# Optimization experiments

Hardware: AMD Instinct MI355X
Metric: run time of the kernel (lower is better)

Reference implementation:

```python
import jax, jax.numpy as jnp
import numpy as np

P = 16  # patch size

def _conv1x1(w, b, h):
    # w: [O, C], h: [B, C, H, W]
    return jnp.einsum('oc,bcij->boij', w, h) + b[None, :, None, None]

def _forward(x, pe_w, pe_b, mix1_w, mix1_b, mix2_w, mix2_b, qc_w, qc_b,
             codebook, dpre1_w, dpre1_b, dpre2_w, dpre2_b, up_w, up_b):
    B, Cin, H, W = x.shape
    Hp, Wp = H // P, W // P
    # --- encoder: non-overlapping patchify conv (kernel=stride=P) ---
    xp = x.reshape(B, Cin, Hp, P, Wp, P)
    h = jnp.einsum('bcipjq,ocpq->boij', xp, pe_w) + pe_b[None, :, None, None]
    h = jax.nn.relu(h)
    h = jax.nn.relu(_conv1x1(mix1_w, mix1_b, h))
    h = _conv1x1(mix2_w, mix2_b, h)
    # quantize_conv_b
    e = _conv1x1(qc_w, qc_b, h)                      # [B, D, Hp, Wp]
    D = e.shape[1]
    z = e.transpose(0, 2, 3, 1).reshape(B, Hp * Wp, D)   # [B, N, D]
    # --- vector quantization: euclidean argmin over codebook ---
    # dist[b,n,k] = |z|^2 - 2 z.c_k + |c_k|^2
    dist = ((z * z).sum(-1, keepdims=True)
            - 2.0 * jnp.einsum('bnd,kd->bnk', z, codebook)
            + (codebook * codebook).sum(-1))
    idx = jnp.argmin(dist, axis=-1)                  # [B, N] int
    q = codebook[idx]                                # [B, N, D]
    # commitment loss (quantize detached, as in VectorQuantize)
    diff = jnp.mean(jnp.square(jax.lax.stop_gradient(q) - z))
    # straight-through estimator
    q = z + jax.lax.stop_gradient(q - z)
    quant = q.reshape(B, Hp, Wp, D).transpose(0, 3, 1, 2)  # [B, D, Hp, Wp]
    # --- decoder ---
    h = jax.nn.relu(_conv1x1(dpre1_w, dpre1_b, quant))
    h = jax.nn.relu(_conv1x1(dpre2_w, dpre2_b, h))
    # unpatchify: ConvTranspose2d kernel=stride=P, torch weight [C, out, P, P]
    Cout = up_w.shape[1]
    dec = jnp.einsum('bcij,copq->boipjq', h, up_w).reshape(B, Cout, Hp * P, Wp * P)
    dec = dec + up_b[None, :, None, None]
    return dec, diff[None], idx

def setup_inputs() -> dict:
    key = jax.random.key(0)
    ks = jax.random.split(key, 16)
    B, Cin, H, W = 32, 3, 256, 256
    C, D, K = 256, 512, 8192
    s = 0.02
    f32 = jnp.float32
    return {
        'x':       jax.random.normal(ks[0], (B, Cin, H, W), f32),
        'pe_w':    jax.random.normal(ks[1], (C, Cin, P, P), f32) * s,
        'pe_b':    jnp.zeros((C,), f32),
        'mix1_w':  jax.random.normal(ks[2], (C, C), f32) * s,
        'mix1_b':  jnp.zeros((C,), f32),
        'mix2_w':  jax.random.normal(ks[3], (C, C), f32) * s,
        'mix2_b':  jnp.zeros((C,), f32),
        'qc_w':    jax.random.normal(ks[4], (D, C), f32) * s,
        'qc_b':    jnp.zeros((D,), f32),
        'codebook': jax.random.normal(ks[5], (K, D), f32),
        'dpre1_w': jax.random.normal(ks[6], (C, D), f32) * s,
        'dpre1_b': jnp.zeros((C,), f32),
        'dpre2_w': jax.random.normal(ks[7], (C, C), f32) * s,
        'dpre2_b': jnp.zeros((C,), f32),
        'up_w':    jax.random.normal(ks[8], (C, Cin, P, P), f32) * s,
        'up_b':    jnp.zeros((Cin,), f32),
    }

def reference(x, pe_w, pe_b, mix1_w, mix1_b, mix2_w, mix2_b, qc_w, qc_b,
              codebook, dpre1_w, dpre1_b, dpre2_w, dpre2_b, up_w, up_b):
    return _forward(x, pe_w, pe_b, mix1_w, mix1_b, mix2_w, mix2_b, qc_w, qc_b,
                    codebook, dpre1_w, dpre1_b, dpre2_w, dpre2_b, up_w, up_b)
```

## Files before the change

kernel.cpp:

```cpp
#include <hip/hip_runtime.h>
#include <hip/hip_bf16.h>
#include <float.h>


#define TOK   8192
#define CBK   8192
#define CBD   512

typedef short  short8v __attribute__((ext_vector_type(8)));
typedef float  f32x4   __attribute__((ext_vector_type(4)));

__device__ __forceinline__ unsigned short f2bf(float x) {
    union { __hip_bfloat16 b; unsigned short u; } c;
    c.b = __float2bfloat16(x);
    return c.u;
}
__device__ __forceinline__ float bf2f(unsigned short h) {
    return __uint_as_float((unsigned)h << 16);
}

template<int NPASS, int AMODE, int STMODE, bool RELU>
__global__ __launch_bounds__(256)
void gemm_mfma(const float* __restrict__ A, const float* __restrict__ Bw,
               const float* __restrict__ bias, float* __restrict__ C,
               const float* __restrict__ rowidx, int M, int N, int K)
{
    __shared__ __align__(16) unsigned short Az[2][128 * 64];
    __shared__ __align__(16) unsigned short Bc[2][64 * 64];

    const int tid = threadIdx.x, lane = tid & 63, wid = tid >> 6;
    const int wr = wid >> 1, wc = wid & 1;
    const int m0 = blockIdx.x * 128, n0 = blockIdx.y * 64;
    const int l15 = lane & 15, l4 = lane >> 4;

    size_t abase[4];
    #pragma unroll
    for (int it = 0; it < 4; ++it) {
        const int m = m0 + it * 32 + (tid >> 3);
        if constexpr (AMODE == 1) {
            const int b = m >> 8, i = (m >> 4) & 15, j = m & 15;
            abase[it] = (size_t)b * 196608 + i * 4096 + j * 16;
        } else if constexpr (AMODE == 2) {
            abase[it] = (size_t)((int)rowidx[m]) * K;
        } else {
            abase[it] = (size_t)m * K;
        }
    }

    f32x4 acc[4][2];
    #pragma unroll
    for (int mi = 0; mi < 4; ++mi)
        #pragma unroll
        for (int nj = 0; nj < 2; ++nj)
            acc[mi][nj] = (f32x4){0.f, 0.f, 0.f, 0.f};

    for (int k0 = 0; k0 < K; k0 += 64) {
        __syncthreads();
        #pragma unroll
        for (int it = 0; it < 4; ++it) {
            const int ci = it * 256 + tid;
            const int r = ci >> 3, cb8 = ci & 7;
            const int kk = k0 + cb8 * 8;
            const float* src;
            if constexpr (AMODE == 1) {
                const int c = kk >> 8, p = (kk >> 4) & 15, q = kk & 15;
                src = A + abase[it] + (size_t)c * 65536 + p * 256 + q;
            } else {
                src = A + abase[it] + kk;
            }
            const float4 f0 = *(const float4*)src;
            const float4 f1 = *(const float4*)(src + 4);
            const float fs[8] = {f0.x, f0.y, f0.z, f0.w, f1.x, f1.y, f1.z, f1.w};
            union { unsigned short u[8]; short8v v; } H, L;
            #pragma unroll
            for (int j = 0; j < 8; ++j) {
                const unsigned short h = f2bf(fs[j]);
                H.u[j] = h;
                L.u[j] = f2bf(fs[j] - bf2f(h));
            }
            const int off = r * 64 + ((cb8 ^ (r & 7)) << 3);
            *(short8v*)(&Az[0][off]) = H.v;
            *(short8v*)(&Az[1][off]) = L.v;
        }
        #pragma unroll
        for (int it = 0; it < 2; ++it) {
            const int ci = it * 256 + tid;
            const int r = ci >> 3, cb8 = ci & 7;
            const float* src = Bw + (size_t)(n0 + r) * K + k0 + cb8 * 8;
            const float4 f0 = *(const float4*)src;
            const float4 f1 = *(const float4*)(src + 4);
            const float fs[8] = {f0.x, f0.y, f0.z, f0.w, f1.x, f1.y, f1.z, f1.w};
            union { unsigned short u[8]; short8v v; } H, L;
            #pragma unroll
            for (int j = 0; j < 8; ++j) {
                const unsigned short h = f2bf(fs[j]);
                H.u[j] = h;
                L.u[j] = f2bf(fs[j] - bf2f(h));
            }
            const int off = r * 64 + ((cb8 ^ (r & 7)) << 3);
            *(short8v*)(&Bc[0][off]) = H.v;
            *(short8v*)(&Bc[1][off]) = L.v;
        }
        __syncthreads();

        #pragma unroll
        for (int ks = 0; ks < 2; ++ks) {
            short8v aFh[4], aFl[4];
            #pragma unroll
            for (int mi = 0; mi < 4; ++mi) {
                const int r = wr * 64 + mi * 16 + l15;
                const int off = r * 64 + (((ks * 4 + l4) ^ (r & 7)) << 3);
                aFh[mi] = *(const short8v*)(&Az[0][off]);
                aFl[mi] = *(const short8v*)(&Az[1][off]);
            }
            #pragma unroll
            for (int nj = 0; nj < 2; ++nj) {
                const int rn = wc * 32 + nj * 16 + l15;
                const int off = rn * 64 + (((ks * 4 + l4) ^ (rn & 7)) << 3);
                const short8v bh = *(const short8v*)(&Bc[0][off]);
                const short8v bl = *(const short8v*)(&Bc[1][off]);
                #pragma unroll
                for (int mi = 0; mi < 4; ++mi) {
                    acc[mi][nj] = __builtin_amdgcn_mfma_f32_16x16x32_bf16(aFh[mi], bh, acc[mi][nj], 0, 0, 0);
                    acc[mi][nj] = __builtin_amdgcn_mfma_f32_16x16x32_bf16(aFh[mi], bl, acc[mi][nj], 0, 0, 0);
                    acc[mi][nj] = __builtin_amdgcn_mfma_f32_16x16x32_bf16(aFl[mi], bh, acc[mi][nj], 0, 0, 0);
                    if constexpr (NPASS == 4)
                        acc[mi][nj] = __builtin_amdgcn_mfma_f32_16x16x32_bf16(aFl[mi], bl, acc[mi][nj], 0, 0, 0);
                }
            }
        }
    }

    #pragma unroll
    for (int nj = 0; nj < 2; ++nj) {
        const int n = n0 + wc * 32 + nj * 16 + l15;
        const float bv = (STMODE == 0) ? bias[n] : bias[n >> 8];
        #pragma unroll
        for (int mi = 0; mi < 4; ++mi) {
            #pragma unroll
            for (int i = 0; i < 4; ++i) {
                const int m = m0 + wr * 64 + mi * 16 + l4 * 4 + i;
                float v = acc[mi][nj][i] + bv;
                if constexpr (RELU) v = fmaxf(v, 0.f);
                if constexpr (STMODE == 0) {
                    C[(size_t)m * N + n] = v;
                } else {
                    const int o = n >> 8, p = (n >> 4) & 15, q = n & 15;
                    const int b = m >> 8, ii = (m >> 4) & 15, jj = m & 15;
                    C[((size_t)(b * 3 + o) * 256 + ii * 16 + p) * 256 + jj * 16 + q] = v;
                }
            }
        }
    }
}

__global__ __launch_bounds__(256)
void cb_norm(const float* __restrict__ cb, float* __restrict__ cnorm)
{
    const int row  = blockIdx.x * 4 + (threadIdx.x >> 6);
    const int lane = threadIdx.x & 63;
    const float4* p = (const float4*)(cb + (size_t)row * CBD + lane * 8);
    const float4 a = p[0], b = p[1];
    double s = (double)a.x*a.x + (double)a.y*a.y + (double)a.z*a.z + (double)a.w*a.w
             + (double)b.x*b.x + (double)b.y*b.y + (double)b.z*b.z + (double)b.w*b.w;
    #pragma unroll
    for (int off = 32; off >= 1; off >>= 1) s += __shfl_down(s, off);
    if (lane == 0) cnorm[row] = (float)s;
}

__global__ __launch_bounds__(256)
void split_bf16_h(const float* __restrict__ src, unsigned short* __restrict__ hi)
{
    const size_t i8 = (size_t)blockIdx.x * 256 + threadIdx.x;
    const float4 a = *(const float4*)(src + i8 * 8);
    const float4 b = *(const float4*)(src + i8 * 8 + 4);
    const float xs[8] = {a.x, a.y, a.z, a.w, b.x, b.y, b.z, b.w};
    union { unsigned short u[8]; short8v v; } H;
    #pragma unroll
    for (int j = 0; j < 8; ++j) H.u[j] = f2bf(xs[j]);
    *(short8v*)(hi + i8 * 8) = H.v;
}

#define NSY 8
#define CPB (CBK / NSY)
#define NCAND 32

__global__ __launch_bounds__(256)
void vq_mfma1(const unsigned short* __restrict__ zh, const unsigned short* __restrict__ cbh,
              const float* __restrict__ cnorm, int* __restrict__ cand)
{
    __shared__ __align__(16) unsigned short Az[128 * 64];
    __shared__ __align__(16) unsigned short Bc[128 * 64];

    const int tid = threadIdx.x, lane = tid & 63, wid = tid >> 6;
    const int wr = wid >> 1, wc = wid & 1;
    const int m0 = blockIdx.x * 128;
    const int l15 = lane & 15, l4 = lane >> 4;

    float r1[16], r2[16];
    int   i1[16], i2[16];
    #pragma unroll
    for (int r = 0; r < 16; ++r) { r1[r] = FLT_MAX; r2[r] = FLT_MAX; i1[r] = 0; i2[r] = 0; }

    for (int chk = 0; chk < CPB / 128; ++chk) {
        const int c0 = blockIdx.y * CPB + chk * 128;

        f32x4 acc[4][4];
        #pragma unroll
        for (int mi = 0; mi < 4; ++mi)
            #pragma unroll
            for (int nj = 0; nj < 4; ++nj)
                acc[mi][nj] = (f32x4){0.f, 0.f, 0.f, 0.f};

        for (int k0 = 0; k0 < CBD; k0 += 64) {
            __syncthreads();
            #pragma unroll
            for (int it = 0; it < 4; ++it) {
                const int ci = it * 256 + tid;
                const int r = ci >> 3, cb8 = ci & 7;
                const int off = r * 64 + ((cb8 ^ (r & 7)) << 3);
                *(short8v*)(&Az[off]) =
                    *(const short8v*)(zh + (size_t)(m0 + r) * CBD + k0 + cb8 * 8);
                *(short8v*)(&Bc[off]) =
                    *(const short8v*)(cbh + (size_t)(c0 + r) * CBD + k0 + cb8 * 8);
            }
            __syncthreads();

            #pragma unroll
            for (int ks = 0; ks < 2; ++ks) {
                short8v aF[4];
                #pragma unroll
                for (int mi = 0; mi < 4; ++mi) {
                    const int r = wr * 64 + mi * 16 + l15;
                    aF[mi] = *(const short8v*)(&Az[r * 64 + (((ks * 4 + l4) ^ (r & 7)) << 3)]);
                }
                #pragma unroll
                for (int nj = 0; nj < 4; ++nj) {
                    const int rn = wc * 64 + nj * 16 + l15;
                    const short8v bF = *(const short8v*)(&Bc[rn * 64 + (((ks * 4 + l4) ^ (rn & 7)) << 3)]);
                    #pragma unroll
                    for (int mi = 0; mi < 4; ++mi)
                        acc[mi][nj] = __builtin_amdgcn_mfma_f32_16x16x32_bf16(aF[mi], bF, acc[mi][nj], 0, 0, 0);
                }
            }
        }

        #pragma unroll
        for (int nj = 0; nj < 4; ++nj) {
            const int code = c0 + wc * 64 + nj * 16 + l15;
            const float cn = cnorm[code];
            #pragma unroll
            for (int mi = 0; mi < 4; ++mi) {
                #pragma unroll
                for (int i = 0; i < 4; ++i) {
                    const float d = cn - 2.0f * acc[mi][nj][i];
                    const int rr = mi * 4 + i;
                    if (d < r1[rr]) { r2[rr] = r1[rr]; i2[rr] = i1[rr]; r1[rr] = d; i1[rr] = code; }
                    else if (d < r2[rr]) { r2[rr] = d; i2[rr] = code; }
                }
            }
        }
    }

    #pragma unroll
    for (int r = 0; r < 16; ++r) {
        float a1 = r1[r], a2 = r2[r];
        int   x1 = i1[r], x2 = i2[r];
        #pragma unroll
        for (int off = 1; off < 16; off <<= 1) {
            const float b1 = __shfl_xor(a1, off), b2 = __shfl_xor(a2, off);
            const int   y1 = __shfl_xor(x1, off), y2 = __shfl_xor(x2, off);
            if (b1 < a1) {
                const float n2 = (a1 < b2) ? a1 : b2;
                const int   m2 = (a1 < b2) ? x1 : y2;
                a2 = n2; x2 = m2; a1 = b1; x1 = y1;
            } else {
                if (b1 < a2) { a2 = b1; x2 = y1; }
            }
        }
        r1[r] = a1; i1[r] = x1; r2[r] = a2; i2[r] = x2;
    }
    if (l15 == 0) {
        const int slot = blockIdx.y * 2 + wc;
        #pragma unroll
        for (int mi = 0; mi < 4; ++mi)
            #pragma unroll
            for (int i = 0; i < 4; ++i) {
                const int tok = m0 + wr * 64 + mi * 16 + l4 * 4 + i;
                cand[(slot * 2 + 0) * TOK + tok] = i1[mi * 4 + i];
                cand[(slot * 2 + 1) * TOK + tok] = i2[mi * 4 + i];
            }
    }
}

__global__ __launch_bounds__(256)
void exact_select(const float* __restrict__ z, const float* __restrict__ cb,
                  const int* __restrict__ cand, int ncand,
                  float* __restrict__ idx_out, float* __restrict__ diffp)
{
    const int t    = blockIdx.x * 4 + (threadIdx.x >> 6);
    const int lane = threadIdx.x & 63;

    const float4 za = *(const float4*)(z + (size_t)t * CBD + lane * 8);
    const float4 zb = *(const float4*)(z + (size_t)t * CBD + lane * 8 + 4);
    const double zd[8] = {za.x, za.y, za.z, za.w, zb.x, zb.y, zb.z, zb.w};

    double bestd = DBL_MAX;
    int    besti = 0x7fffffff;
    for (int c = 0; c < ncand; ++c) {
        const int code = cand[c * TOK + t];
        const float4 ca  = *(const float4*)(cb + (size_t)code * CBD + lane * 8);
        const float4 cbv = *(const float4*)(cb + (size_t)code * CBD + lane * 8 + 4);
        const double cd[8] = {ca.x, ca.y, ca.z, ca.w, cbv.x, cbv.y, cbv.z, cbv.w};
        double s = 0.0;
        #pragma unroll
        for (int j = 0; j < 8; ++j) { const double d = cd[j] - zd[j]; s = fma(d, d, s); }
        #pragma unroll
        for (int off = 32; off >= 1; off >>= 1) s += __shfl_down(s, off);
        s = __shfl(s, 0);
        if (s < bestd || (s == bestd && code < besti)) { bestd = s; besti = code; }
    }
    if (lane == 0) {
        idx_out[t] = (float)besti;
        atomicAdd(diffp, (float)(bestd * (1.0 / ((double)TOK * CBD))));
    }
}

__global__ __launch_bounds__(256)
void transpose_upw(const float* __restrict__ up_w, float* __restrict__ upT)
{
    const int id = blockIdx.x * 256 + threadIdx.x;
    const int n = id >> 8, c = id & 255;
    upT[id] = up_w[c * 768 + n];
}

extern "C" void kernel_launch(void* const* d_in, const int* in_sizes, int n_in,
                              void* d_out, int out_size, void* d_ws, size_t ws_size,
                              hipStream_t stream)
{
    const float* x        = (const float*)d_in[0];
    const float* pe_w     = (const float*)d_in[1];
    const float* pe_b     = (const float*)d_in[2];
    const float* mix1_w   = (const float*)d_in[3];
    const float* mix1_b   = (const float*)d_in[4];
    const float* mix2_w   = (const float*)d_in[5];
    const float* mix2_b   = (const float*)d_in[6];
    const float* qc_w     = (const float*)d_in[7];
    const float* qc_b     = (const float*)d_in[8];
    const float* codebook = (const float*)d_in[9];
    const float* dpre1_w  = (const float*)d_in[10];
    const float* dpre1_b  = (const float*)d_in[11];
    const float* dpre2_w  = (const float*)d_in[12];
    const float* dpre2_b  = (const float*)d_in[13];
    const float* up_w     = (const float*)d_in[14];
    const float* up_b     = (const float*)d_in[15];

    float* ws = (float*)d_ws;
    float* h1    = ws;
    float* h2    = ws + 2097152;
    float* z     = ws + 4194304;
    float* upT   = ws + 8388608;
    float* cnorm = ws + 8585216;
    int*   cand  = (int*)(ws + 8593408);
    unsigned short* zh  = (unsigned short*)(ws + 8855552);
    unsigned short* cbh = (unsigned short*)(ws + 10952704);

    float* dec     = (float*)d_out;
    float* diffp   = dec + 6291456;
    float* idx_out = (float*)d_out + 6291457;

    transpose_upw<<<768, 256, 0, stream>>>(up_w, upT);
    cb_norm<<<CBK / 4, 256, 0, stream>>>(codebook, cnorm);
    split_bf16_h<<<2048, 256, 0, stream>>>(codebook, cbh);

    gemm_mfma<4, 1, 0, true ><<<dim3(64, 4),  256, 0, stream>>>(x,  pe_w,   pe_b,   h1, nullptr, TOK, 256, 768);
    gemm_mfma<4, 0, 0, true ><<<dim3(64, 4),  256, 0, stream>>>(h1, mix1_w, mix1_b, h2, nullptr, TOK, 256, 256);
    gemm_mfma<4, 0, 0, false><<<dim3(64, 4),  256, 0, stream>>>(h2, mix2_w, mix2_b, h1, nullptr, TOK, 256, 256);
    gemm_mfma<4, 0, 0, false><<<dim3(64, 8),  256, 0, stream>>>(h1, qc_w,   qc_b,   z,  nullptr, TOK, 512, 256);

    split_bf16_h<<<2048, 256, 0, stream>>>(z, zh);
    vq_mfma1<<<dim3(TOK / 128, NSY), 256, 0, stream>>>(zh, cbh, cnorm, cand);
    hipMemsetAsync(diffp, 0, sizeof(float), stream);
    exact_select<<<TOK / 4, 256, 0, stream>>>(z, codebook, cand, NCAND, idx_out, diffp);

    gemm_mfma<3, 2, 0, true ><<<dim3(64, 4),  256, 0, stream>>>(codebook, dpre1_w, dpre1_b, h1, idx_out, TOK, 256, 512);
    gemm_mfma<3, 0, 0, true ><<<dim3(64, 4),  256, 0, stream>>>(h1, dpre2_w, dpre2_b, h2, nullptr, TOK, 256, 256);
    gemm_mfma<3, 0, 1, false><<<dim3(64, 12), 256, 0, stream>>>(h2, upT, up_b, dec, nullptr, TOK, 768, 256);
}
```

Measured before the change: 720.7 us.

## Pre-split operands to bf16 hi/lo and double-buffer GEMMs with direct global-to-LDS loads

```diff
diff --git a/kernel.cpp b/kernel.cpp
--- a/kernel.cpp
+++ b/kernel.cpp
@@ -9,6 +9,7 @@
 
 typedef short  short8v __attribute__((ext_vector_type(8)));
 typedef float  f32x4   __attribute__((ext_vector_type(4)));
+typedef unsigned short ush;
 
 __device__ __forceinline__ unsigned short f2bf(float x) {
     union { __hip_bfloat16 b; unsigned short u; } c;
@@ -19,33 +20,65 @@
     return __uint_as_float((unsigned)h << 16);
 }
 
+__device__ __forceinline__ void gload16(const void* g, void* l) {
+    __builtin_amdgcn_global_load_lds(
+        (const __attribute__((address_space(1))) unsigned int*)g,
+        (__attribute__((address_space(3))) unsigned int*)l, 16, 0, 0);
+}
+
 template<int NPASS, int AMODE, int STMODE, bool RELU>
 __global__ __launch_bounds__(256)
-void gemm_mfma(const float* __restrict__ A, const float* __restrict__ Bw,
-               const float* __restrict__ bias, float* __restrict__ C,
-               const float* __restrict__ rowidx, int M, int N, int K)
-{
-    __shared__ __align__(16) unsigned short Az[2][128 * 64];
-    __shared__ __align__(16) unsigned short Bc[2][64 * 64];
+void gemm_bf2(const ush* __restrict__ Ah, const ush* __restrict__ Al,
+              const ush* __restrict__ Bh, const ush* __restrict__ Bl,
+              const float* __restrict__ bias,
+              float* __restrict__ Cf, ush* __restrict__ Ch, ush* __restrict__ Cl,
+              const float* __restrict__ rowidx, int N, int K, int NT)
+{
+    __shared__ __align__(16) ush AzH[2][128 * 64];
+    __shared__ __align__(16) ush AzL[2][128 * 64];
+    __shared__ __align__(16) ush BcH[2][64 * 64];
+    __shared__ __align__(16) ush BcL[2][64 * 64];
 
     const int tid = threadIdx.x, lane = tid & 63, wid = tid >> 6;
     const int wr = wid >> 1, wc = wid & 1;
     const int m0 = blockIdx.x * 128, n0 = blockIdx.y * 64;
     const int l15 = lane & 15, l4 = lane >> 4;
 
-    size_t abase[4];
-    #pragma unroll
-    for (int it = 0; it < 4; ++it) {
-        const int m = m0 + it * 32 + (tid >> 3);
-        if constexpr (AMODE == 1) {
-            const int b = m >> 8, i = (m >> 4) & 15, j = m & 15;
-            abase[it] = (size_t)b * 196608 + i * 4096 + j * 16;
-        } else if constexpr (AMODE == 2) {
-            abase[it] = (size_t)((int)rowidx[m]) * K;
-        } else {
-            abase[it] = (size_t)m * K;
-        }
-    }
+    size_t aoff[4];
+    int    aldst[4];
+    #pragma unroll
+    for (int i = 0; i < 4; ++i) {
+        const int ci = (wid * 4 + i) * 64 + lane;
+        const int r = ci >> 3, p = ci & 7;
+        size_t rowbase;
+        if constexpr (AMODE == 2) rowbase = (size_t)((int)rowidx[m0 + r]) * K;
+        else                      rowbase = (size_t)(m0 + r) * K;
+        aoff[i]  = rowbase + ((p ^ (r & 7)) << 3);
+        aldst[i] = (wid * 4 + i) * 512;
+    }
+    size_t boff[2];
+    int    bldst[2];
+    #pragma unroll
+    for (int i = 0; i < 2; ++i) {
+        const int ci = (wid * 2 + i) * 64 + lane;
+        const int r = ci >> 3, p = ci & 7;
+        boff[i]  = (size_t)(n0 + r) * K + ((p ^ (r & 7)) << 3);
+        bldst[i] = (wid * 2 + i) * 512;
+    }
+
+    auto STAGE = [&](int t, int b) {
+        const int k0 = t << 6;
+        #pragma unroll
+        for (int i = 0; i < 4; ++i) {
+            gload16(Ah + aoff[i] + k0, &AzH[b][aldst[i]]);
+            gload16(Al + aoff[i] + k0, &AzL[b][aldst[i]]);
+        }
+        #pragma unroll
+        for (int i = 0; i < 2; ++i) {
+            gload16(Bh + boff[i] + k0, &BcH[b][bldst[i]]);
+            gload16(Bl + boff[i] + k0, &BcL[b][bldst[i]]);
+        }
+    };
 
     f32x4 acc[4][2];
     #pragma unroll
@@ -54,55 +87,11 @@
         for (int nj = 0; nj < 2; ++nj)
             acc[mi][nj] = (f32x4){0.f, 0.f, 0.f, 0.f};
 
-    for (int k0 = 0; k0 < K; k0 += 64) {
-        __syncthreads();
-        #pragma unroll
-        for (int it = 0; it < 4; ++it) {
-            const int ci = it * 256 + tid;
-            const int r = ci >> 3, cb8 = ci & 7;
-            const int kk = k0 + cb8 * 8;
-            const float* src;
-            if constexpr (AMODE == 1) {
-                const int c = kk >> 8, p = (kk >> 4) & 15, q = kk & 15;
-                src = A + abase[it] + (size_t)c * 65536 + p * 256 + q;
-            } else {
-                src = A + abase[it] + kk;
-            }
-            const float4 f0 = *(const float4*)src;
-            const float4 f1 = *(const float4*)(src + 4);
-            const float fs[8] = {f0.x, f0.y, f0.z, f0.w, f1.x, f1.y, f1.z, f1.w};
-            union { unsigned short u[8]; short8v v; } H, L;
-            #pragma unroll
-            for (int j = 0; j < 8; ++j) {
-                const unsigned short h = f2bf(fs[j]);
-                H.u[j] = h;
-                L.u[j] = f2bf(fs[j] - bf2f(h));
-            }
-            const int off = r * 64 + ((cb8 ^ (r & 7)) << 3);
-            *(short8v*)(&Az[0][off]) = H.v;
-            *(short8v*)(&Az[1][off]) = L.v;
-        }
-        #pragma unroll
-        for (int it = 0; it < 2; ++it) {
-            const int ci = it * 256 + tid;
-            const int r = ci >> 3, cb8 = ci & 7;
-            const float* src = Bw + (size_t)(n0 + r) * K + k0 + cb8 * 8;
-            const float4 f0 = *(const float4*)src;
-            const float4 f1 = *(const float4*)(src + 4);
-            const float fs[8] = {f0.x, f0.y, f0.z, f0.w, f1.x, f1.y, f1.z, f1.w};
-            union { unsigned short u[8]; short8v v; } H, L;
-            #pragma unroll
-            for (int j = 0; j < 8; ++j) {
-                const unsigned short h = f2bf(fs[j]);
-                H.u[j] = h;
-                L.u[j] = f2bf(fs[j] - bf2f(h));
-            }
-            const int off = r * 64 + ((cb8 ^ (r & 7)) << 3);
-            *(short8v*)(&Bc[0][off]) = H.v;
-            *(short8v*)(&Bc[1][off]) = L.v;
-        }
-        __syncthreads();
-
+    STAGE(0, 0);
+    __syncthreads();
+    for (int t = 0; t < NT; ++t) {
+        const int b = t & 1;
+        if (t + 1 < NT) STAGE(t + 1, b ^ 1);
         #pragma unroll
         for (int ks = 0; ks < 2; ++ks) {
             short8v aFh[4], aFl[4];
@@ -110,15 +99,15 @@
             for (int mi = 0; mi < 4; ++mi) {
                 const int r = wr * 64 + mi * 16 + l15;
                 const int off = r * 64 + (((ks * 4 + l4) ^ (r & 7)) << 3);
-                aFh[mi] = *(const short8v*)(&Az[0][off]);
-                aFl[mi] = *(const short8v*)(&Az[1][off]);
+                aFh[mi] = *(const short8v*)(&AzH[b][off]);
+                aFl[mi] = *(const short8v*)(&AzL[b][off]);
             }
             #pragma unroll
             for (int nj = 0; nj < 2; ++nj) {
                 const int rn = wc * 32 + nj * 16 + l15;
                 const int off = rn * 64 + (((ks * 4 + l4) ^ (rn & 7)) << 3);
-                const short8v bh = *(const short8v*)(&Bc[0][off]);
-                const short8v bl = *(const short8v*)(&Bc[1][off]);
+                const short8v bh = *(const short8v*)(&BcH[b][off]);
+                const short8v bl = *(const short8v*)(&BcL[b][off]);
                 #pragma unroll
                 for (int mi = 0; mi < 4; ++mi) {
                     acc[mi][nj] = __builtin_amdgcn_mfma_f32_16x16x32_bf16(aFh[mi], bh, acc[mi][nj], 0, 0, 0);
@@ -129,12 +118,13 @@
                 }
             }
         }
+        __syncthreads();
     }
 
     #pragma unroll
     for (int nj = 0; nj < 2; ++nj) {
         const int n = n0 + wc * 32 + nj * 16 + l15;
-        const float bv = (STMODE == 0) ? bias[n] : bias[n >> 8];
+        const float bv = (STMODE == 2) ? bias[n >> 8] : bias[n];
         #pragma unroll
         for (int mi = 0; mi < 4; ++mi) {
             #pragma unroll
@@ -143,11 +133,16 @@
                 float v = acc[mi][nj][i] + bv;
                 if constexpr (RELU) v = fmaxf(v, 0.f);
                 if constexpr (STMODE == 0) {
-                    C[(size_t)m * N + n] = v;
+                    const unsigned short h = f2bf(v);
+                    Ch[(size_t)m * N + n] = h;
+                    Cl[(size_t)m * N + n] = f2bf(v - bf2f(h));
+                } else if constexpr (STMODE == 1) {
+                    Cf[(size_t)m * N + n] = v;
+                    Ch[(size_t)m * N + n] = f2bf(v);
                 } else {
                     const int o = n >> 8, p = (n >> 4) & 15, q = n & 15;
-                    const int b = m >> 8, ii = (m >> 4) & 15, jj = m & 15;
-                    C[((size_t)(b * 3 + o) * 256 + ii * 16 + p) * 256 + jj * 16 + q] = v;
+                    const int b2 = m >> 8, ii = (m >> 4) & 15, jj = m & 15;
+                    Cf[((size_t)(b2 * 3 + o) * 256 + ii * 16 + p) * 256 + jj * 16 + q] = v;
                 }
             }
         }
@@ -155,111 +150,93 @@
 }
 
 __global__ __launch_bounds__(256)
-void cb_norm(const float* __restrict__ cb, float* __restrict__ cnorm)
-{
-    const int row  = blockIdx.x * 4 + (threadIdx.x >> 6);
-    const int lane = threadIdx.x & 63;
-    const float4* p = (const float4*)(cb + (size_t)row * CBD + lane * 8);
-    const float4 a = p[0], b = p[1];
-    double s = (double)a.x*a.x + (double)a.y*a.y + (double)a.z*a.z + (double)a.w*a.w
-             + (double)b.x*b.x + (double)b.y*b.y + (double)b.z*b.z + (double)b.w*b.w;
-    #pragma unroll
-    for (int off = 32; off >= 1; off >>= 1) s += __shfl_down(s, off);
-    if (lane == 0) cnorm[row] = (float)s;
-}
-
-__global__ __launch_bounds__(256)
-void split_bf16_h(const float* __restrict__ src, unsigned short* __restrict__ hi)
-{
-    const size_t i8 = (size_t)blockIdx.x * 256 + threadIdx.x;
-    const float4 a = *(const float4*)(src + i8 * 8);
-    const float4 b = *(const float4*)(src + i8 * 8 + 4);
-    const float xs[8] = {a.x, a.y, a.z, a.w, b.x, b.y, b.z, b.w};
-    union { unsigned short u[8]; short8v v; } H;
-    #pragma unroll
-    for (int j = 0; j < 8; ++j) H.u[j] = f2bf(xs[j]);
-    *(short8v*)(hi + i8 * 8) = H.v;
-}
-
-#define NSY 8
-#define CPB (CBK / NSY)
-#define NCAND 32
-
-__global__ __launch_bounds__(256)
-void vq_mfma1(const unsigned short* __restrict__ zh, const unsigned short* __restrict__ cbh,
-              const float* __restrict__ cnorm, int* __restrict__ cand)
-{
-    __shared__ __align__(16) unsigned short Az[128 * 64];
-    __shared__ __align__(16) unsigned short Bc[128 * 64];
+void vq_scan(const ush* __restrict__ zh, const ush* __restrict__ cbh,
+             const float* __restrict__ cnorm, int* __restrict__ cand)
+{
+    __shared__ __align__(16) ush Az[2][128 * 64];
+    __shared__ __align__(16) ush Bc[2][128 * 64];
 
     const int tid = threadIdx.x, lane = tid & 63, wid = tid >> 6;
     const int wr = wid >> 1, wc = wid & 1;
     const int m0 = blockIdx.x * 128;
+    const int cy = blockIdx.y;
     const int l15 = lane & 15, l4 = lane >> 4;
+
+    size_t soff[4];
+    int    ldst[4];
+    #pragma unroll
+    for (int i = 0; i < 4; ++i) {
+        const int ci = (wid * 4 + i) * 64 + lane;
+        const int r = ci >> 3, p = ci & 7;
+        soff[i] = (size_t)r * CBD + ((p ^ (r & 7)) << 3);
+        ldst[i] = (wid * 4 + i) * 512;
+    }
+
+    auto STAGE = [&](int t, int b) {
+        const int chk = t >> 3, k0 = (t & 7) << 6;
+        const size_t ab = (size_t)m0 * CBD + k0;
+        const size_t bb = (size_t)(cy * 1024 + chk * 128) * CBD + k0;
+        #pragma unroll
+        for (int i = 0; i < 4; ++i) {
+            gload16(zh  + ab + soff[i], &Az[b][ldst[i]]);
+            gload16(cbh + bb + soff[i], &Bc[b][ldst[i]]);
+        }
+    };
 
     float r1[16], r2[16];
     int   i1[16], i2[16];
     #pragma unroll
     for (int r = 0; r < 16; ++r) { r1[r] = FLT_MAX; r2[r] = FLT_MAX; i1[r] = 0; i2[r] = 0; }
 
-    for (int chk = 0; chk < CPB / 128; ++chk) {
-        const int c0 = blockIdx.y * CPB + chk * 128;
-
-        f32x4 acc[4][4];
-        #pragma unroll
-        for (int mi = 0; mi < 4; ++mi)
-            #pragma unroll
-            for (int nj = 0; nj < 4; ++nj)
-                acc[mi][nj] = (f32x4){0.f, 0.f, 0.f, 0.f};
-
-        for (int k0 = 0; k0 < CBD; k0 += 64) {
-            __syncthreads();
-            #pragma unroll
-            for (int it = 0; it < 4; ++it) {
-                const int ci = it * 256 + tid;
-                const int r = ci >> 3, cb8 = ci & 7;
-                const int off = r * 64 + ((cb8 ^ (r & 7)) << 3);
-                *(short8v*)(&Az[off]) =
-                    *(const short8v*)(zh + (size_t)(m0 + r) * CBD + k0 + cb8 * 8);
-                *(short8v*)(&Bc[off]) =
-                    *(const short8v*)(cbh + (size_t)(c0 + r) * CBD + k0 + cb8 * 8);
-            }
-            __syncthreads();
-
-            #pragma unroll
-            for (int ks = 0; ks < 2; ++ks) {
-                short8v aF[4];
+    f32x4 acc[4][4];
+    STAGE(0, 0);
+    __syncthreads();
+    for (int t = 0; t < 64; ++t) {
+        const int b = t & 1;
+        if (t < 63) STAGE(t + 1, b ^ 1);
+        if ((t & 7) == 0) {
+            #pragma unroll
+            for (int mi = 0; mi < 4; ++mi)
+                #pragma unroll
+                for (int nj = 0; nj < 4; ++nj)
+                    acc[mi][nj] = (f32x4){0.f, 0.f, 0.f, 0.f};
+        }
+        #pragma unroll
+        for (int ks = 0; ks < 2; ++ks) {
+            short8v aF[4];
+            #pragma unroll
+            for (int mi = 0; mi < 4; ++mi) {
+                const int r = wr * 64 + mi * 16 + l15;
+                aF[mi] = *(const short8v*)(&Az[b][r * 64 + (((ks * 4 + l4) ^ (r & 7)) << 3)]);
+            }
+            #pragma unroll
+            for (int nj = 0; nj < 4; ++nj) {
+                const int rn = wc * 64 + nj * 16 + l15;
+                const short8v bF = *(const short8v*)(&Bc[b][rn * 64 + (((ks * 4 + l4) ^ (rn & 7)) << 3)]);
+                #pragma unroll
+                for (int mi = 0; mi < 4; ++mi)
+                    acc[mi][nj] = __builtin_amdgcn_mfma_f32_16x16x32_bf16(aF[mi], bF, acc[mi][nj], 0, 0, 0);
+            }
+        }
+        if ((t & 7) == 7) {
+            const int c0 = cy * 1024 + (t >> 3) * 128;
+            #pragma unroll
+            for (int nj = 0; nj < 4; ++nj) {
+                const int code = c0 + wc * 64 + nj * 16 + l15;
+                const float cn = cnorm[code];
                 #pragma unroll
                 for (int mi = 0; mi < 4; ++mi) {
-                    const int r = wr * 64 + mi * 16 + l15;
-                    aF[mi] = *(const short8v*)(&Az[r * 64 + (((ks * 4 + l4) ^ (r & 7)) << 3)]);
+                    #pragma unroll
+                    for (int i = 0; i < 4; ++i) {
+                        const float d = cn - 2.0f * acc[mi][nj][i];
+                        const int rr = mi * 4 + i;
+                        if (d < r1[rr]) { r2[rr] = r1[rr]; i2[rr] = i1[rr]; r1[rr] = d; i1[rr] = code; }
+                        else if (d < r2[rr]) { r2[rr] = d; i2[rr] = code; }
+                    }
                 }
-                #pragma unroll
-                for (int nj = 0; nj < 4; ++nj) {
-                    const int rn = wc * 64 + nj * 16 + l15;
-                    const short8v bF = *(const short8v*)(&Bc[rn * 64 + (((ks * 4 + l4) ^ (rn & 7)) << 3)]);
-                    #pragma unroll
-                    for (int mi = 0; mi < 4; ++mi)
-                        acc[mi][nj] = __builtin_amdgcn_mfma_f32_16x16x32_bf16(aF[mi], bF, acc[mi][nj], 0, 0, 0);
-                }
-            }
-        }
-
-        #pragma unroll
-        for (int nj = 0; nj < 4; ++nj) {
-            const int code = c0 + wc * 64 + nj * 16 + l15;
-            const float cn = cnorm[code];
-            #pragma unroll
-            for (int mi = 0; mi < 4; ++mi) {
-                #pragma unroll
-                for (int i = 0; i < 4; ++i) {
-                    const float d = cn - 2.0f * acc[mi][nj][i];
-                    const int rr = mi * 4 + i;
-                    if (d < r1[rr]) { r2[rr] = r1[rr]; i2[rr] = i1[rr]; r1[rr] = d; i1[rr] = code; }
-                    else if (d < r2[rr]) { r2[rr] = d; i2[rr] = code; }
-                }
-            }
-        }
+            }
+        }
+        __syncthreads();
     }
 
     #pragma unroll
@@ -281,7 +258,7 @@
         r1[r] = a1; i1[r] = x1; r2[r] = a2; i2[r] = x2;
     }
     if (l15 == 0) {
-        const int slot = blockIdx.y * 2 + wc;
+        const int slot = cy * 2 + wc;
         #pragma unroll
         for (int mi = 0; mi < 4; ++mi)
             #pragma unroll
@@ -327,11 +304,68 @@
 }
 
 __global__ __launch_bounds__(256)
-void transpose_upw(const float* __restrict__ up_w, float* __restrict__ upT)
+void cb_norm(const float* __restrict__ cb, float* __restrict__ cnorm)
+{
+    const int row  = blockIdx.x * 4 + (threadIdx.x >> 6);
+    const int lane = threadIdx.x & 63;
+    const float4* p = (const float4*)(cb + (size_t)row * CBD + lane * 8);
+    const float4 a = p[0], b = p[1];
+    double s = (double)a.x*a.x + (double)a.y*a.y + (double)a.z*a.z + (double)a.w*a.w
+             + (double)b.x*b.x + (double)b.y*b.y + (double)b.z*b.z + (double)b.w*b.w;
+    #pragma unroll
+    for (int off = 32; off >= 1; off >>= 1) s += __shfl_down(s, off);
+    if (lane == 0) cnorm[row] = (float)s;
+}
+
+__global__ __launch_bounds__(256)
+void split_hl(const float* __restrict__ src, ush* __restrict__ h, ush* __restrict__ l)
+{
+    const size_t i8 = (size_t)blockIdx.x * 256 + threadIdx.x;
+    const float4 a = *(const float4*)(src + i8 * 8);
+    const float4 b = *(const float4*)(src + i8 * 8 + 4);
+    const float xs[8] = {a.x, a.y, a.z, a.w, b.x, b.y, b.z, b.w};
+    union { unsigned short u[8]; short8v v; } H, L;
+    #pragma unroll
+    for (int j = 0; j < 8; ++j) {
+        const unsigned short hh = f2bf(xs[j]);
+        H.u[j] = hh;
+        L.u[j] = f2bf(xs[j] - bf2f(hh));
+    }
+    *(short8v*)(h + i8 * 8) = H.v;
+    *(short8v*)(l + i8 * 8) = L.v;
+}
+
+__global__ __launch_bounds__(256)
+void split_x(const float* __restrict__ x, ush* __restrict__ xh, ush* __restrict__ xl)
+{
+    const int i8 = blockIdx.x * 256 + threadIdx.x;
+    const int m = i8 / 96, kc = (i8 % 96) * 8;
+    const int b = m >> 8, ii = (m >> 4) & 15, jj = m & 15;
+    const int c = kc >> 8, p = (kc >> 4) & 15, q = kc & 15;
+    const float* src = x + ((size_t)(b * 3 + c) * 256 + ii * 16 + p) * 256 + jj * 16 + q;
+    const float4 a = *(const float4*)src;
+    const float4 d = *(const float4*)(src + 4);
+    const float xs[8] = {a.x, a.y, a.z, a.w, d.x, d.y, d.z, d.w};
+    union { unsigned short u[8]; short8v v; } H, L;
+    #pragma unroll
+    for (int j = 0; j < 8; ++j) {
+        const unsigned short hh = f2bf(xs[j]);
+        H.u[j] = hh;
+        L.u[j] = f2bf(xs[j] - bf2f(hh));
+    }
+    *(short8v*)(xh + (size_t)i8 * 8) = H.v;
+    *(short8v*)(xl + (size_t)i8 * 8) = L.v;
+}
+
+__global__ __launch_bounds__(256)
+void transpose_upw_split(const float* __restrict__ up_w, ush* __restrict__ th, ush* __restrict__ tl)
 {
     const int id = blockIdx.x * 256 + threadIdx.x;
     const int n = id >> 8, c = id & 255;
-    upT[id] = up_w[c * 768 + n];
+    const float v = up_w[c * 768 + n];
+    const unsigned short h = f2bf(v);
+    th[id] = h;
+    tl[id] = f2bf(v - bf2f(h));
 }
 
 extern "C" void kernel_launch(void* const* d_in, const int* in_sizes, int n_in,
@@ -355,35 +389,59 @@
     const float* up_w     = (const float*)d_in[14];
     const float* up_b     = (const float*)d_in[15];
 
-    float* ws = (float*)d_ws;
-    float* h1    = ws;
-    float* h2    = ws + 2097152;
-    float* z     = ws + 4194304;
-    float* upT   = ws + 8388608;
-    float* cnorm = ws + 8585216;
-    int*   cand  = (int*)(ws + 8593408);
-    unsigned short* zh  = (unsigned short*)(ws + 8855552);
-    unsigned short* cbh = (unsigned short*)(ws + 10952704);
+    char* W = (char*)d_ws;
+    ush*   hAh  = (ush*)(W + 0);
+    ush*   hAl  = (ush*)(W + 4194304);
+    ush*   hBh  = (ush*)(W + 8388608);
+    ush*   hBl  = (ush*)(W + 12582912);
+    ush*   xph  = (ush*)(W + 16777216);
+    ush*   xpl  = (ush*)(W + 29360128);
+    float* z    = (float*)(W + 16777216);
+    ush*   zh   = (ush*)(W + 33554432);
+    ush*   cbh  = (ush*)(W + 41943040);
+    ush*   cbl  = (ush*)(W + 50331648);
+    ush*   peh  = (ush*)(W + 58720256);
+    ush*   pel  = (ush*)(W + 59113472);
+    ush*   m1h  = (ush*)(W + 59506688);
+    ush*   m1l  = (ush*)(W + 59637760);
+    ush*   m2h  = (ush*)(W + 59768832);
+    ush*   m2l  = (ush*)(W + 59899904);
+    ush*   qch  = (ush*)(W + 60030976);
+    ush*   qcl  = (ush*)(W + 60293120);
+    ush*   d1h  = (ush*)(W + 60555264);
+    ush*   d1l  = (ush*)(W + 60817408);
+    ush*   d2h  = (ush*)(W + 61079552);
+    ush*   d2l  = (ush*)(W + 61210624);
+    ush*   uTh  = (ush*)(W + 61341696);
+    ush*   uTl  = (ush*)(W + 61734912);
+    float* cnorm= (float*)(W + 62128128);
+    int*   cand = (int*)(W + 62160896);
 
     float* dec     = (float*)d_out;
     float* diffp   = dec + 6291456;
     float* idx_out = (float*)d_out + 6291457;
 
-    transpose_upw<<<768, 256, 0, stream>>>(up_w, upT);
-    cb_norm<<<CBK / 4, 256, 0, stream>>>(codebook, cnorm);
-    split_bf16_h<<<2048, 256, 0, stream>>>(codebook, cbh);
-
-    gemm_mfma<4, 1, 0, true ><<<dim3(64, 4),  256, 0, stream>>>(x,  pe_w,   pe_b,   h1, nullptr, TOK, 256, 768);
-    gemm_mfma<4, 0, 0, true ><<<dim3(64, 4),  256, 0, stream>>>(h1, mix1_w, mix1_b, h2, nullptr, TOK, 256, 256);
-    gemm_mfma<4, 0, 0, false><<<dim3(64, 4),  256, 0, stream>>>(h2, mix2_w, mix2_b, h1, nullptr, TOK, 256, 256);
-    gemm_mfma<4, 0, 0, false><<<dim3(64, 8),  256, 0, stream>>>(h1, qc_w,   qc_b,   z,  nullptr, TOK, 512, 256);
-
-    split_bf16_h<<<2048, 256, 0, stream>>>(z, zh);
-    vq_mfma1<<<dim3(TOK / 128, NSY), 256, 0, stream>>>(zh, cbh, cnorm, cand);
+    split_hl<<<96,   256, 0, stream>>>(pe_w,    peh, pel);
+    split_hl<<<32,   256, 0, stream>>>(mix1_w,  m1h, m1l);
+    split_hl<<<32,   256, 0, stream>>>(mix2_w,  m2h, m2l);
+    split_hl<<<64,   256, 0, stream>>>(qc_w,    qch, qcl);
+    split_hl<<<64,   256, 0, stream>>>(dpre1_w, d1h, d1l);
+    split_hl<<<32,   256, 0, stream>>>(dpre2_w, d2h, d2l);
+    split_hl<<<2048, 256, 0, stream>>>(codebook, cbh, cbl);
+    split_x<<<3072,  256, 0, stream>>>(x, xph, xpl);
+    transpose_upw_split<<<768, 256, 0, stream>>>(up_w, uTh, uTl);
+    cb_norm<<<2048, 256, 0, stream>>>(codebook, cnorm);
+
+    gemm_bf2<4, 0, 0, true ><<<dim3(64, 4),  256, 0, stream>>>(xph, xpl, peh, pel, pe_b,   nullptr, hAh, hAl, nullptr, 256, 768, 12);
+    gemm_bf2<4, 0, 0, true ><<<dim3(64, 4),  256, 0, stream>>>(hAh, hAl, m1h, m1l, mix1_b, nullptr, hBh, hBl, nullptr, 256, 256, 4);
+    gemm_bf2<4, 0, 0, false><<<dim3(64, 4),  256, 0, stream>>>(hBh, hBl, m2h, m2l, mix2_b, nullptr, hAh, hAl, nullptr, 256, 256, 4);
+    gemm_bf2<4, 0, 1, false><<<dim3(64, 8),  256, 0, stream>>>(hAh, hAl, qch, qcl, qc_b,   z,       zh,  nullptr, nullptr, 512, 256, 4);
+
+    vq_scan<<<dim3(64, 8), 256, 0, stream>>>(zh, cbh, cnorm, cand);
     hipMemsetAsync(diffp, 0, sizeof(float), stream);
-    exact_select<<<TOK / 4, 256, 0, stream>>>(z, codebook, cand, NCAND, idx_out, diffp);
-
-    gemm_mfma<3, 2, 0, true ><<<dim3(64, 4),  256, 0, stream>>>(codebook, dpre1_w, dpre1_b, h1, idx_out, TOK, 256, 512);
-    gemm_mfma<3, 0, 0, true ><<<dim3(64, 4),  256, 0, stream>>>(h1, dpre2_w, dpre2_b, h2, nullptr, TOK, 256, 256);
-    gemm_mfma<3, 0, 1, false><<<dim3(64, 12), 256, 0, stream>>>(h2, upT, up_b, dec, nullptr, TOK, 768, 256);
-}
+    exact_select<<<TOK / 4, 256, 0, stream>>>(z, codebook, cand, 32, idx_out, diffp);
+
+    gemm_bf2<3, 2, 0, true ><<<dim3(64, 4),  256, 0, stream>>>(cbh, cbl, d1h, d1l, dpre1_b, nullptr, hAh, hAl, idx_out, 256, 512, 8);
+    gemm_bf2<3, 0, 0, true ><<<dim3(64, 4),  256, 0, stream>>>(hAh, hAl, d2h, d2l, dpre2_b, nullptr, hBh, hBl, nullptr, 256, 256, 4);
+    gemm_bf2<3, 0, 2, false><<<dim3(64, 12), 256, 0, stream>>>(hBh, hBl, uTh, uTl, up_b,    dec,     nullptr, nullptr, nullptr, 768, 256, 4);
+}
```

After: 722.1 us. About the same (+0.2%).
